# Optimization experiments

Measured on AMD Instinct MI355X. Metric: run time of the kernel, lower is better.

## Reference

```python
import jax, jax.numpy as jnp
import numpy as np

D_Q = D_K = D_V = 1024
H = 16
D_ATT = 64
NQ = NK = 4096
EPS = 1e-12


def setup_inputs() -> dict:
    key = jax.random.key(0)
    ks = jax.random.split(key, 12)
    s_in = 1.0 / np.sqrt(D_Q)
    s_out = 1.0 / np.sqrt(H * D_ATT)
    return {
        "queries": jax.random.normal(ks[0], (NQ, D_Q), jnp.float32),
        "keys": jax.random.normal(ks[1], (NK, D_K), jnp.float32),
        "values": jax.random.normal(ks[2], (NK, D_V), jnp.float32),
        "Wq": jax.random.uniform(ks[3], (D_Q, H * D_ATT), jnp.float32, -s_in, s_in),
        "bq": jax.random.uniform(ks[4], (H * D_ATT,), jnp.float32, -s_in, s_in),
        "Wk": jax.random.uniform(ks[5], (D_K, H * D_ATT), jnp.float32, -s_in, s_in),
        "bk": jax.random.uniform(ks[6], (H * D_ATT,), jnp.float32, -s_in, s_in),
        "Wv": jax.random.uniform(ks[7], (D_V, H * D_ATT), jnp.float32, -s_in, s_in),
        "bv": jax.random.uniform(ks[8], (H * D_ATT,), jnp.float32, -s_in, s_in),
        "Wo": jax.random.uniform(ks[9], (H * D_ATT, D_Q), jnp.float32, -s_out, s_out),
        "bo": jax.random.uniform(ks[10], (D_Q,), jnp.float32, -s_out, s_out),
        "gamma": jnp.ones((D_Q,), jnp.float32),
        "beta": jnp.zeros((D_Q,), jnp.float32),
    }


def reference(queries, keys, values, Wq, bq, Wk, bk, Wv, bv, Wo, bo, gamma, beta):
    nq = queries.shape[0]
    nk = keys.shape[0]
    # projections -> (n, h, d)
    q = (queries @ Wq + bq).reshape(nq, H, D_ATT)
    k = (keys @ Wk + bk).reshape(nk, H, D_ATT)
    v = (values @ Wv + bv).reshape(nk, H, D_ATT)
    # scores (h, nq, nk)
    att = jnp.einsum("qhd,khd->hqk", q, k) / np.sqrt(D_ATT).astype(np.float32)
    att = jax.nn.softmax(att, axis=-1)  # dropout = identity (eval)
    out = jnp.einsum("hqk,khd->qhd", att, v).reshape(nq, H * D_ATT)
    out = queries + out @ Wo + bo
    # LayerNorm, eps=1e-12
    mu = jnp.mean(out, axis=-1, keepdims=True)
    var = jnp.mean(jnp.square(out - mu), axis=-1, keepdims=True)
    out = (out - mu) * jax.lax.rsqrt(var + EPS) * gamma + beta
    return out
```

## Files before the change

### kernel.cpp

```cpp
#include <hip/hip_runtime.h>
#include <stdint.h>

typedef unsigned short u16;
typedef unsigned int u32;
typedef __attribute__((ext_vector_type(8))) __bf16 bf16x8;
typedef __attribute__((ext_vector_type(2))) __bf16 bf16x2;
typedef __attribute__((ext_vector_type(4))) float f32x4;
typedef __attribute__((ext_vector_type(16))) float f32x16;
typedef __attribute__((ext_vector_type(8))) u16 u16x8;
typedef __attribute__((ext_vector_type(4))) u32 u32x4;

#define Q_SCALE 0.1803368801111204f

__device__ __forceinline__ float ex2(float x) { return __builtin_amdgcn_exp2f(x); }

__device__ __forceinline__ u16 f2bf(float f) {
  __bf16 h = (__bf16)f;
  return __builtin_bit_cast(u16, h);
}
__device__ __forceinline__ float bf2f(u16 u) {
  u32 x = ((u32)u) << 16;
  return __builtin_bit_cast(float, x);
}
__device__ __forceinline__ u32 pack2(float a, float b) {
  bf16x2 v; v.x = (__bf16)a; v.y = (__bf16)b;
  return __builtin_bit_cast(u32, v);
}
__device__ __forceinline__ void gl_lds16(const void* g, void* l) {
  __builtin_amdgcn_global_load_lds((const __attribute__((address_space(1))) void*)g,
                                   (__attribute__((address_space(3))) void*)l, 16, 0, 0);
}

__global__ __launch_bounds__(256) void prep_kernel(const float* __restrict__ Wq,
                                                   const float* __restrict__ Wk,
                                                   const float* __restrict__ Wv,
                                                   const float* __restrict__ Wo,
                                                   u16* __restrict__ wcatT,
                                                   u16* __restrict__ woT) {
  __shared__ u16 tile[64][72];
  int z = blockIdx.z;
  int t = threadIdx.x;
  const float* W = z == 0 ? Wq : z == 1 ? Wk : z == 2 ? Wv : Wo;
  int k0 = blockIdx.y * 64, n0 = blockIdx.x * 64;
  int r = t >> 2, c0 = (t & 3) * 16;
  const float* src = W + (size_t)(k0 + r) * 1024 + n0 + c0;
#pragma unroll
  for (int i = 0; i < 16; i += 4) {
    float4 x = *(const float4*)(src + i);
    tile[r][c0 + i] = f2bf(x.x); tile[r][c0 + i + 1] = f2bf(x.y);
    tile[r][c0 + i + 2] = f2bf(x.z); tile[r][c0 + i + 3] = f2bf(x.w);
  }
  __syncthreads();
  int n = t >> 2, kc = (t & 3) * 16;
  u16x8 o0, o1;
#pragma unroll
  for (int j = 0; j < 8; ++j) { o0[j] = tile[kc + j][n]; o1[j] = tile[kc + 8 + j][n]; }
  u16* dst = (z < 3) ? (wcatT + (size_t)z * 1048576 + (size_t)(n0 + n) * 1024 + k0 + kc)
                     : (woT + (size_t)(n0 + n) * 1024 + k0 + kc);
  *(u16x8*)dst = o0;
  *(u16x8*)(dst + 8) = o1;
}

__global__ __launch_bounds__(512) void gemm_bt(const float* __restrict__ Aq,
                                               const float* __restrict__ Ak,
                                               const float* __restrict__ Av,
                                               const u16* __restrict__ BT,
                                               u16* __restrict__ outBF,
                                               const float* __restrict__ b0,
                                               const float* __restrict__ b1,
                                               const float* __restrict__ b2) {
  __shared__ u16 As[2][4096];
  __shared__ u16 Bs[2][4096];
  int tid = threadIdx.x;
  int bid = blockIdx.y * 8 + blockIdx.x;
  int cpx = gridDim.y;
  int swz = (bid & 7) * cpx + (bid >> 3);
  int m0 = (swz >> 3) * 128, n0 = (swz & 7) * 128;
  int sec = m0 >> 12;
  const float* A32 = sec == 0 ? Aq : sec == 1 ? Ak : Av;
  int mbase = m0 & 4095;
  const u16* bt = BT + (size_t)sec * 1048576;
  int w = tid >> 6, l = tid & 63;
  int wr = w >> 1, wc = w & 1;
  f32x4 acc[2][4];
#pragma unroll
  for (int i = 0; i < 2; ++i)
#pragma unroll
    for (int j = 0; j < 4; ++j)
#pragma unroll
      for (int rr = 0; rr < 4; ++rr) acc[i][j][rr] = 0.f;

  int rS = tid >> 2, cpS = tid & 3;
  int clS = cpS ^ ((rS ^ (rS >> 2)) & 3);
  const float* srcA = A32 + (size_t)(mbase + rS) * 1024 + clS * 8;
  const u16* srcB = bt + (size_t)(n0 + rS) * 1024 + clS * 8;
  int dstS = tid * 8;
  float4 pa, pb4;
  auto loadA = [&](int kt) {
    pa = *(const float4*)(srcA + kt * 32);
    pb4 = *(const float4*)(srcA + kt * 32 + 4);
  };
  auto writeA = [&](int buf) {
    u16x8 o;
    o[0] = f2bf(pa.x); o[1] = f2bf(pa.y); o[2] = f2bf(pa.z); o[3] = f2bf(pa.w);
    o[4] = f2bf(pb4.x); o[5] = f2bf(pb4.y); o[6] = f2bf(pb4.z); o[7] = f2bf(pb4.w);
    *(u16x8*)&As[buf][dstS] = o;
  };
  auto stageB = [&](int buf, int kt) {
    gl_lds16(srcB + kt * 32, &Bs[buf][dstS]);
  };
  loadA(0);
  stageB(0, 0);
  writeA(0);
  __syncthreads();
  int sw = (l & 3) ^ ((l >> 2) & 3);
  int phys = (l >> 4) ^ sw;
  for (int kt = 0; kt < 32; ++kt) {
    int buf = kt & 1;
    if (kt < 31) {
      loadA(kt + 1);
      stageB(buf ^ 1, kt + 1);
    }
    bf16x8 af[2], bfr[4];
#pragma unroll
    for (int mi = 0; mi < 2; ++mi) {
      int row = wr * 32 + mi * 16 + (l & 15);
      af[mi] = *(const bf16x8*)&As[buf][row * 32 + phys * 8];
    }
#pragma unroll
    for (int nj = 0; nj < 4; ++nj) {
      int rowb = wc * 64 + nj * 16 + (l & 15);
      bfr[nj] = *(const bf16x8*)&Bs[buf][rowb * 32 + phys * 8];
    }
#pragma unroll
    for (int mi = 0; mi < 2; ++mi)
#pragma unroll
      for (int nj = 0; nj < 4; ++nj)
        acc[mi][nj] = __builtin_amdgcn_mfma_f32_16x16x32_bf16(af[mi], bfr[nj],
                                                              acc[mi][nj], 0, 0, 0);
    if (kt < 31) writeA(buf ^ 1);
    __syncthreads();
  }
  const float* bp = sec == 0 ? b0 : sec == 1 ? b1 : b2;
#pragma unroll
  for (int mi = 0; mi < 2; ++mi)
#pragma unroll
    for (int nj = 0; nj < 4; ++nj)
#pragma unroll
      for (int rr = 0; rr < 4; ++rr) {
        int orow = mbase + wr * 32 + mi * 16 + (l >> 4) * 4 + rr;
        int col = n0 + wc * 64 + nj * 16 + (l & 15);
        float vv = acc[mi][nj][rr] + bp[col];
        if (sec == 0) vv *= Q_SCALE;
        outBF[(size_t)sec * 4194304 + (size_t)orow * 1024 + col] = f2bf(vv);
      }
}

__global__ __launch_bounds__(512) void gemm_n64(const u16* __restrict__ A,
                                                const u16* __restrict__ BT,
                                                float* __restrict__ outF,
                                                const float* __restrict__ b0,
                                                const float* __restrict__ resid) {
  __shared__ u16 As[2][4096];
  __shared__ u16 Bs[2][2048];
  int tid = threadIdx.x;
  int bid = blockIdx.y * 8 + blockIdx.x;
  int swz = (bid & 7) * 64 + (bid >> 3);
  int m0 = (swz >> 4) * 128, n0 = (swz & 15) * 64;
  int w = tid >> 6, l = tid & 63;
  int wr = w >> 1, wc = w & 1;
  f32x4 acc[2][2];
#pragma unroll
  for (int i = 0; i < 2; ++i)
#pragma unroll
    for (int j = 0; j < 2; ++j)
#pragma unroll
      for (int rr = 0; rr < 4; ++rr) acc[i][j][rr] = 0.f;

  int rS = tid >> 2, cpS = tid & 3;
  int clS = cpS ^ ((rS ^ (rS >> 2)) & 3);
  const u16* srcA = A + (size_t)(m0 + rS) * 1024 + clS * 8;
  const u16* srcB = BT + (size_t)(n0 + rS) * 1024 + clS * 8;
  int dstS = tid * 8;
  auto stage = [&](int buf, int kt) {
    gl_lds16(srcA + kt * 32, &As[buf][dstS]);
    if (tid < 256) gl_lds16(srcB + kt * 32, &Bs[buf][dstS]);
  };
  stage(0, 0);
  __syncthreads();
  int sw = (l & 3) ^ ((l >> 2) & 3);
  int phys = (l >> 4) ^ sw;
  for (int kt = 0; kt < 32; ++kt) {
    int buf = kt & 1;
    if (kt < 31) stage(buf ^ 1, kt + 1);
    bf16x8 af[2], bfr[2];
#pragma unroll
    for (int mi = 0; mi < 2; ++mi) {
      int row = wr * 32 + mi * 16 + (l & 15);
      af[mi] = *(const bf16x8*)&As[buf][row * 32 + phys * 8];
    }
#pragma unroll
    for (int nj = 0; nj < 2; ++nj) {
      int rowb = wc * 32 + nj * 16 + (l & 15);
      bfr[nj] = *(const bf16x8*)&Bs[buf][rowb * 32 + phys * 8];
    }
#pragma unroll
    for (int mi = 0; mi < 2; ++mi)
#pragma unroll
      for (int nj = 0; nj < 2; ++nj)
        acc[mi][nj] = __builtin_amdgcn_mfma_f32_16x16x32_bf16(af[mi], bfr[nj],
                                                              acc[mi][nj], 0, 0, 0);
    __syncthreads();
  }
#pragma unroll
  for (int mi = 0; mi < 2; ++mi)
#pragma unroll
    for (int nj = 0; nj < 2; ++nj)
#pragma unroll
      for (int rr = 0; rr < 4; ++rr) {
        int row = m0 + wr * 32 + mi * 16 + (l >> 4) * 4 + rr;
        int col = n0 + wc * 32 + nj * 16 + (l & 15);
        outF[(size_t)row * 1024 + col] =
            acc[mi][nj][rr] + b0[col] + resid[(size_t)row * 1024 + col];
      }
}

__global__ __launch_bounds__(256) void vtrans_kernel(const u16* __restrict__ vp,
                                                     u16* __restrict__ vt) {
  __shared__ u16 tile[64][72];
  int t = threadIdx.x;
  int n0 = blockIdx.x * 64, h = blockIdx.y;
  int r = t >> 2, c0 = (t & 3) * 16;
  u16x8 a = *(const u16x8*)(vp + (size_t)(n0 + r) * 1024 + h * 64 + c0);
  u16x8 b = *(const u16x8*)(vp + (size_t)(n0 + r) * 1024 + h * 64 + c0 + 8);
#pragma unroll
  for (int j = 0; j < 8; ++j) { tile[r][c0 + j] = a[j]; tile[r][c0 + 8 + j] = b[j]; }
  __syncthreads();
  int d = t >> 2, nc = (t & 3) * 16;
  u16x8 o0, o1;
#pragma unroll
  for (int j = 0; j < 8; ++j) { o0[j] = tile[nc + j][d]; o1[j] = tile[nc + 8 + j][d]; }
  size_t base = (size_t)(h * 64 + d) * 4096 + n0 + nc;
  *(u16x8*)(vt + base) = o0;
  *(u16x8*)(vt + base + 8) = o1;
}

__global__ __launch_bounds__(512, 4) void attn_kernel(const u16* __restrict__ qp,
                                                      const u16* __restrict__ kp,
                                                      const u16* __restrict__ vt,
                                                      u16* __restrict__ attout) {
  __shared__ u16 smem[32768];
  int tid = threadIdx.x;
  int w = tid >> 6, l = tid & 63;
  int half = w >> 2, wl = w & 3;
  int hi = l >> 5, l31 = l & 31;
  int h = blockIdx.y, bx = blockIdx.x;
  int qrow = bx * 128 + wl * 32 + l31;
  bf16x8 qf[4];
#pragma unroll
  for (int ds = 0; ds < 4; ++ds)
    qf[ds] = *(const bf16x8*)(qp + (size_t)qrow * 1024 + h * 64 + ds * 16 + hi * 8);

  f32x16 zero16;
#pragma unroll
  for (int r = 0; r < 16; ++r) zero16[r] = 0.f;
  f32x16 accO[2];
#pragma unroll
  for (int r = 0; r < 16; ++r) { accO[0][r] = 0.f; accO[1][r] = 0.f; }
  float l_run = 0.f;

  u16* sbase = smem + half * 16384;
  int ht = (wl << 6) | l;
  const u16* srcK[2]; const u16* srcV[2]; int dstOff[2];
#pragma unroll
  for (int i = 0; i < 2; ++i) {
    int id = i * 256 + ht;
    int r = id >> 3, cp = id & 7;
    int cl = cp ^ ((r ^ (r >> 3)) & 7);
    srcK[i] = kp + (size_t)(half * 2048 + r) * 1024 + h * 64 + cl * 8;
    srcV[i] = vt + (size_t)(h * 64 + r) * 4096 + half * 2048 + cl * 8;
    dstOff[i] = id * 8;
  }
  auto stage = [&](int buf, int kt) {
    u16* b = sbase + buf * 8192;
#pragma unroll
    for (int i = 0; i < 2; ++i) {
      gl_lds16(srcK[i] + (size_t)kt * 65536, b + dstOff[i]);
      gl_lds16(srcV[i] + kt * 64, b + 4096 + dstOff[i]);
    }
  };
  stage(0, 0);
  __syncthreads();

  for (int kt = 0; kt < 32; ++kt) {
    int buf = kt & 1;
    if (kt < 31) stage(buf ^ 1, kt + 1);
    const u16* Kt = sbase + buf * 8192;
    const u16* Vt = Kt + 4096;

    f32x16 accS[2];
    __builtin_amdgcn_s_setprio(1);
#pragma unroll
    for (int mt = 0; mt < 2; ++mt) {
      int row = mt * 32 + l31;
      int g = (row ^ (row >> 3)) & 7;
      {
        bf16x8 kf = *(const bf16x8*)(Kt + row * 64 + ((0 + hi) ^ g) * 8);
        accS[mt] = __builtin_amdgcn_mfma_f32_32x32x16_bf16(kf, qf[0], zero16, 0, 0, 0);
      }
#pragma unroll
      for (int ds = 1; ds < 4; ++ds) {
        int phys = (2 * ds + hi) ^ g;
        bf16x8 kf = *(const bf16x8*)(Kt + row * 64 + phys * 8);
        accS[mt] = __builtin_amdgcn_mfma_f32_32x32x16_bf16(kf, qf[ds], accS[mt], 0, 0, 0);
      }
    }
    __builtin_amdgcn_s_setprio(0);

    u32 pku[2][8];
    float s0 = 0.f, s1 = 0.f, s2 = 0.f, s3 = 0.f;
#pragma unroll
    for (int mt = 0; mt < 2; ++mt)
#pragma unroll
      for (int qd = 0; qd < 8; ++qd) {
        float a = ex2(accS[mt][2 * qd]);
        float b = ex2(accS[mt][2 * qd + 1]);
        if (qd & 1) { s2 += a; s3 += b; } else { s0 += a; s1 += b; }
        pku[mt][qd] = pack2(a, b);
      }
    l_run += (s0 + s1) + (s2 + s3);

    bf16x8 pb[4];
#pragma unroll
    for (int ks = 0; ks < 4; ++ks) {
      const int mt = ks >> 1, k1 = ks & 1;
      u32 a0 = pku[mt][4 * k1 + 0], c0 = pku[mt][4 * k1 + 2];
      u32 a1 = pku[mt][4 * k1 + 1], c1 = pku[mt][4 * k1 + 3];
      asm("v_permlane32_swap_b32 %0, %1" : "+v"(a0), "+v"(c0));
      asm("v_permlane32_swap_b32 %0, %1" : "+v"(a1), "+v"(c1));
      u32x4 fr;
      fr[0] = a0; fr[1] = a1; fr[2] = c0; fr[3] = c1;
      pb[ks] = __builtin_bit_cast(bf16x8, fr);
    }
    __builtin_amdgcn_s_setprio(1);
#pragma unroll
    for (int mto = 0; mto < 2; ++mto) {
      int row = mto * 32 + l31;
      int g = (row ^ (row >> 3)) & 7;
#pragma unroll
      for (int ks = 0; ks < 4; ++ks) {
        int phys = (2 * ks + hi) ^ g;
        bf16x8 vf = *(const bf16x8*)(Vt + row * 64 + phys * 8);
        accO[mto] = __builtin_amdgcn_mfma_f32_32x32x16_bf16(vf, pb[ks], accO[mto], 0, 0, 0);
      }
    }
    __builtin_amdgcn_s_setprio(0);
    __syncthreads();
  }
  l_run += __shfl_xor(l_run, 32, 64);

  u16* pO = smem;
  float* ml = (float*)(smem + 2 * 128 * 72);
  int q = wl * 32 + l31;
#pragma unroll
  for (int mto = 0; mto < 2; ++mto)
#pragma unroll
    for (int g = 0; g < 4; ++g)
#pragma unroll
      for (int j = 0; j < 2; ++j) {
        int r = g * 4 + j * 2;
        int d = j * 2 + 8 * g + 4 * hi + 32 * mto;
        u32 pk = pack2(accO[mto][r], accO[mto][r + 1]);
        *(u32*)&pO[(size_t)(half * 128 + q) * 72 + d] = pk;
      }
  if (hi == 0) ml[half * 128 + q] = l_run;
  __syncthreads();
  {
    int qq = tid >> 2, d0 = (tid & 3) * 16;
    float invL = 1.f / (ml[qq] + ml[128 + qq]);
    u16x8 ra0 = *(u16x8*)&pO[(size_t)qq * 72 + d0];
    u16x8 ra1 = *(u16x8*)&pO[(size_t)qq * 72 + d0 + 8];
    u16x8 rb0 = *(u16x8*)&pO[(size_t)(128 + qq) * 72 + d0];
    u16x8 rb1 = *(u16x8*)&pO[(size_t)(128 + qq) * 72 + d0 + 8];
    u16x8 o0, o1;
#pragma unroll
    for (int j = 0; j < 8; ++j) {
      o0[j] = f2bf((bf2f(ra0[j]) + bf2f(rb0[j])) * invL);
      o1[j] = f2bf((bf2f(ra1[j]) + bf2f(rb1[j])) * invL);
    }
    size_t ob = (size_t)(bx * 128 + qq) * 1024 + (size_t)h * 64 + d0;
    *(u16x8*)(attout + ob) = o0;
    *(u16x8*)(attout + ob + 8) = o1;
  }
}

__global__ __launch_bounds__(256) void ln_kernel(float* __restrict__ io,
                                                 const float* __restrict__ gamma,
                                                 const float* __restrict__ beta) {
  int row = blockIdx.x, t = threadIdx.x;
  float4 v = *(const float4*)(io + (size_t)row * 1024 + t * 4);
  float s = v.x + v.y + v.z + v.w;
  float sq = v.x * v.x + v.y * v.y + v.z * v.z + v.w * v.w;
#pragma unroll
  for (int off = 1; off < 64; off <<= 1) {
    s += __shfl_xor(s, off, 64);
    sq += __shfl_xor(sq, off, 64);
  }
  __shared__ float rs[4], rq[4];
  if ((t & 63) == 0) { rs[t >> 6] = s; rq[t >> 6] = sq; }
  __syncthreads();
  float S = rs[0] + rs[1] + rs[2] + rs[3];
  float Q = rq[0] + rq[1] + rq[2] + rq[3];
  float mu = S * (1.f / 1024.f);
  float var = Q * (1.f / 1024.f) - mu * mu;
  float invs = rsqrtf(var + 1e-12f);
  float4 g = *(const float4*)(gamma + t * 4);
  float4 b = *(const float4*)(beta + t * 4);
  float4 o;
  o.x = (v.x - mu) * invs * g.x + b.x;
  o.y = (v.y - mu) * invs * g.y + b.y;
  o.z = (v.z - mu) * invs * g.z + b.z;
  o.w = (v.w - mu) * invs * g.w + b.w;
  *(float4*)(io + (size_t)row * 1024 + t * 4) = o;
}

extern "C" void kernel_launch(void* const* d_in, const int* in_sizes, int n_in,
                              void* d_out, int out_size, void* d_ws, size_t ws_size,
                              hipStream_t stream) {
  (void)in_sizes; (void)n_in; (void)out_size; (void)ws_size;
  const float* queries = (const float*)d_in[0];
  const float* keys    = (const float*)d_in[1];
  const float* values  = (const float*)d_in[2];
  const float* Wq = (const float*)d_in[3];
  const float* bq = (const float*)d_in[4];
  const float* Wk = (const float*)d_in[5];
  const float* bk = (const float*)d_in[6];
  const float* Wv = (const float*)d_in[7];
  const float* bv = (const float*)d_in[8];
  const float* Wo = (const float*)d_in[9];
  const float* bo = (const float*)d_in[10];
  const float* gamma = (const float*)d_in[11];
  const float* beta  = (const float*)d_in[12];
  float* out = (float*)d_out;

  u16* ws = (u16*)d_ws;
  u16* attout = ws;
  u16* vt     = ws + 4194304;
  u16* wcatT  = ws + 12582912;
  u16* woT    = ws + 15728640;
  u16* qp     = ws + 16777216;
  u16* kp     = qp + 4194304;
  u16* vp     = qp + 8388608;

  prep_kernel<<<dim3(16, 16, 4), dim3(256), 0, stream>>>(Wq, Wk, Wv, Wo, wcatT, woT);
  gemm_bt<<<dim3(8, 96), dim3(512), 0, stream>>>(queries, keys, values, wcatT, qp,
                                                 bq, bk, bv);
  vtrans_kernel<<<dim3(64, 16), dim3(256), 0, stream>>>(vp, vt);
  attn_kernel<<<dim3(32, 16), dim3(512), 0, stream>>>(qp, kp, vt, attout);
  gemm_n64<<<dim3(8, 64), dim3(512), 0, stream>>>(attout, woT, out, bo, queries);
  ln_kernel<<<dim3(4096), dim3(256), 0, stream>>>(out, gamma, beta);
}
```

Before: 160.3 us.

## Software-pipeline PV matmul one tile behind QK to overlap exp with MFMA

Restructures the attention inner loop so the P·V MFMAs for tile kt-1 are issued right after the QK^T MFMAs for tile kt, before the exp/pack of tile kt. K and V are now staged into separate double buffers, with V for tile kt loaded in the same iteration. The aim is to hide softmax exp latency behind matrix work and shorten the dependency chain per iteration. It keeps the pb fragments live across iterations, which adds register pressure, and it needs an epilogue to finish the last tile.

```diff
diff --git a/kernel.cpp b/kernel.cpp
--- a/kernel.cpp
+++ b/kernel.cpp
@@ -281,22 +281,27 @@
     srcV[i] = vt + (size_t)(h * 64 + r) * 4096 + half * 2048 + cl * 8;
     dstOff[i] = id * 8;
   }
-  auto stage = [&](int buf, int kt) {
-    u16* b = sbase + buf * 8192;
-#pragma unroll
-    for (int i = 0; i < 2; ++i) {
+  auto stageK = [&](int buf, int kt) {
+    u16* b = sbase + buf * 4096;
+#pragma unroll
+    for (int i = 0; i < 2; ++i)
       gl_lds16(srcK[i] + (size_t)kt * 65536, b + dstOff[i]);
-      gl_lds16(srcV[i] + kt * 64, b + 4096 + dstOff[i]);
-    }
-  };
-  stage(0, 0);
-  __syncthreads();
-
+  };
+  auto stageV = [&](int buf, int kt) {
+    u16* b = sbase + 8192 + buf * 4096;
+#pragma unroll
+    for (int i = 0; i < 2; ++i)
+      gl_lds16(srcV[i] + kt * 64, b + dstOff[i]);
+  };
+  stageK(0, 0);
+  __syncthreads();
+
+  bf16x8 pb[4];
   for (int kt = 0; kt < 32; ++kt) {
-    int buf = kt & 1;
-    if (kt < 31) stage(buf ^ 1, kt + 1);
-    const u16* Kt = sbase + buf * 8192;
-    const u16* Vt = Kt + 4096;
+    int kb = kt & 1;
+    if (kt < 31) stageK(kb ^ 1, kt + 1);
+    stageV(kb, kt);
+    const u16* Kt = sbase + kb * 4096;
 
     f32x16 accS[2];
     __builtin_amdgcn_s_setprio(1);
@@ -315,6 +320,20 @@
         accS[mt] = __builtin_amdgcn_mfma_f32_32x32x16_bf16(kf, qf[ds], accS[mt], 0, 0, 0);
       }
     }
+    if (kt > 0) {
+      const u16* Vt = sbase + 8192 + ((kt - 1) & 1) * 4096;
+#pragma unroll
+      for (int mto = 0; mto < 2; ++mto) {
+        int row = mto * 32 + l31;
+        int g = (row ^ (row >> 3)) & 7;
+#pragma unroll
+        for (int ks = 0; ks < 4; ++ks) {
+          int phys = (2 * ks + hi) ^ g;
+          bf16x8 vf = *(const bf16x8*)(Vt + row * 64 + phys * 8);
+          accO[mto] = __builtin_amdgcn_mfma_f32_32x32x16_bf16(vf, pb[ks], accO[mto], 0, 0, 0);
+        }
+      }
+    }
     __builtin_amdgcn_s_setprio(0);
 
     u32 pku[2][8];
@@ -329,8 +348,6 @@
         pku[mt][qd] = pack2(a, b);
       }
     l_run += (s0 + s1) + (s2 + s3);
-
-    bf16x8 pb[4];
 #pragma unroll
     for (int ks = 0; ks < 4; ++ks) {
       const int mt = ks >> 1, k1 = ks & 1;
@@ -342,6 +359,10 @@
       fr[0] = a0; fr[1] = a1; fr[2] = c0; fr[3] = c1;
       pb[ks] = __builtin_bit_cast(bf16x8, fr);
     }
+    __syncthreads();
+  }
+  {
+    const u16* Vt = sbase + 8192 + (31 & 1) * 4096;
     __builtin_amdgcn_s_setprio(1);
 #pragma unroll
     for (int mto = 0; mto < 2; ++mto) {
@@ -355,9 +376,9 @@
       }
     }
     __builtin_amdgcn_s_setprio(0);
-    __syncthreads();
   }
   l_run += __shfl_xor(l_run, 32, 64);
+  __syncthreads();
 
   u16* pO = smem;
   float* ml = (float*)(smem + 2 * 128 * 72);
```

New measurement: 162.0 us. Within noise of the previous version (+1.0%).
